# Kernel tuning notes

Hardware: AMD Instinct MI355X
Metric: run time of the kernel (lower is better)

## Reference

```python
import jax, jax.numpy as jnp
import numpy as np

TEMPERATURE = 1.0  # module default current_temperature
TOP_K = 2
NUM_EXPERTS = 64
EPS = 1e-10


def setup_inputs() -> dict:
    key = jax.random.key(0)
    k1, k2 = jax.random.split(key)
    x = jax.random.normal(k1, (4, 4096, 2048), dtype=jnp.float32)
    # nn.Linear(d_model, num_experts) weight has shape [num_experts, d_model]
    W_gate = jax.random.normal(k2, (NUM_EXPERTS, 2048), dtype=jnp.float32) * (1.0 / np.sqrt(2048))
    return {"x": x, "W_gate": W_gate}


def reference(x, W_gate):
    # Gate GEMM: [B,S,D] x [E,D] -> [B,S,E]
    logits = jnp.einsum("bsd,ed->bse", x, W_gate)
    scaled = logits / TEMPERATURE
    # Full distribution over experts (for load-balancing loss)
    router_probs = jax.nn.softmax(scaled, axis=-1)
    # Top-k selection over the expert dim, then renormalize via softmax
    top_k_logits, top_k_indices = jax.lax.top_k(scaled, TOP_K)  # [B,S,K]
    top_k_weights = jax.nn.softmax(top_k_logits, axis=-1)
    # Routing stats (no-grad in torch; plain values here)
    entropy = -jnp.sum(router_probs * jnp.log(router_probs + EPS), axis=-1)
    routing_entropy = entropy.mean()
    selection_confidence = top_k_weights[:, :, 0].mean()
    counts = jnp.zeros((NUM_EXPERTS,), dtype=x.dtype).at[top_k_indices.reshape(-1)].add(1.0)
    expert_utilization = counts / (counts.sum() + EPS)
    return (top_k_weights, top_k_indices, router_probs,
            routing_entropy, selection_confidence, expert_utilization)
```

## Files before the change

kernel.cpp:

```cpp
#include <hip/hip_runtime.h>
#include <math.h>

#define NTOK 16384
#define DIM 2048
#define NEXP 64
#define TB 32
#define NSTAGE 64

#define OFF_W    0
#define OFF_I    32768
#define OFF_P    65536
#define OFF_ENT  1114112
#define OFF_CONF 1114113
#define OFF_UTIL 1114114

typedef short s16x8 __attribute__((ext_vector_type(8)));
typedef float f32x4 __attribute__((ext_vector_type(4)));

__device__ __forceinline__ unsigned short f2bf(float v) {
    unsigned u = __builtin_bit_cast(unsigned, v);
    u = u + 0x7FFFu + ((u >> 16) & 1u);
    return (unsigned short)(u >> 16);
}
__device__ __forceinline__ float bf2f(unsigned short b) {
    return __builtin_bit_cast(float, (unsigned)b << 16);
}

__global__ void router_init(float* __restrict__ out) {
    int tid = threadIdx.x;
    if (tid < 66) out[OFF_ENT + tid] = 0.0f;
}

__global__ void router_wsplit(const float* __restrict__ Wg, uint4* __restrict__ wsp) {
    const int c = blockIdx.x;
    const int t = threadIdx.x;
    const int nt = t >> 6, l = t & 63;
    const int e  = 16 * nt + (l & 15);
    const int k0 = 32 * c + 8 * (l >> 4);
    const float* src = Wg + (size_t)e * DIM + k0;
    float4 a = *(const float4*)src;
    float4 b = *(const float4*)(src + 4);
    float v[8] = {a.x, a.y, a.z, a.w, b.x, b.y, b.z, b.w};
    unsigned short H[8], M[8], L[8];
    #pragma unroll
    for (int j = 0; j < 8; ++j) {
        H[j] = f2bf(v[j]);  float r = v[j] - bf2f(H[j]);
        M[j] = f2bf(r);     r = r - bf2f(M[j]);
        L[j] = f2bf(r);
    }
    uint4 ph, pm, pl;
    ph.x = H[0] | ((unsigned)H[1] << 16); ph.y = H[2] | ((unsigned)H[3] << 16);
    ph.z = H[4] | ((unsigned)H[5] << 16); ph.w = H[6] | ((unsigned)H[7] << 16);
    pm.x = M[0] | ((unsigned)M[1] << 16); pm.y = M[2] | ((unsigned)M[3] << 16);
    pm.z = M[4] | ((unsigned)M[5] << 16); pm.w = M[6] | ((unsigned)M[7] << 16);
    pl.x = L[0] | ((unsigned)L[1] << 16); pl.y = L[2] | ((unsigned)L[3] << 16);
    pl.z = L[4] | ((unsigned)L[5] << 16); pl.w = L[6] | ((unsigned)L[7] << 16);
    const int idx = c * 256 + t;
    wsp[idx]         = ph;
    wsp[16384 + idx] = pm;
    wsp[32768 + idx] = pl;
}

#define LOADW(W_, c_) { const int b_ = (c_)*256 + np*128 + l;  \
    W_[0] = wq[b_];          W_[1] = wq[b_ + 64];              \
    W_[2] = wq[16384 + b_];  W_[3] = wq[16384 + b_ + 64];      \
    W_[4] = wq[32768 + b_];  W_[5] = wq[32768 + b_ + 64]; }

#define SPLIT8(a0_, a1_, ph_, pm_, pl_) {                                \
    float xv[8] = {a0_.x, a0_.y, a0_.z, a0_.w,                           \
                   a1_.x, a1_.y, a1_.z, a1_.w};                          \
    unsigned hw_[8], mw_[8], lw_[8];                                     \
    _Pragma("unroll")                                                    \
    for (int j = 0; j < 8; ++j) {                                        \
        unsigned u_  = __builtin_bit_cast(unsigned, xv[j]);              \
        unsigned hb_ = u_ & 0xFFFF0000u;                                 \
        float    r_  = xv[j] - __builtin_bit_cast(float, hb_);           \
        unsigned mb_ = __builtin_bit_cast(unsigned, r_) & 0xFFFF0000u;   \
        float    r2_ = r_ - __builtin_bit_cast(float, mb_);              \
        unsigned lb_ = __builtin_bit_cast(unsigned, r2_);                \
        hw_[j] = hb_ >> 16; mw_[j] = mb_ >> 16; lw_[j] = lb_ >> 16;      \
    }                                                                    \
    ph_.x = hw_[0] | (hw_[1] << 16); ph_.y = hw_[2] | (hw_[3] << 16);    \
    ph_.z = hw_[4] | (hw_[5] << 16); ph_.w = hw_[6] | (hw_[7] << 16);    \
    pm_.x = mw_[0] | (mw_[1] << 16); pm_.y = mw_[2] | (mw_[3] << 16);    \
    pm_.z = mw_[4] | (mw_[5] << 16); pm_.w = mw_[6] | (mw_[7] << 16);    \
    pl_.x = lw_[0] | (lw_[1] << 16); pl_.y = lw_[2] | (lw_[3] << 16);    \
    pl_.z = lw_[4] | (lw_[5] << 16); pl_.w = lw_[6] | (lw_[7] << 16);    \
}

#define STAGEW(buf_) {                                                   \
    uint4 ph_, pm_, pl_;                                                 \
    SPLIT8(xr0, xr1, ph_, pm_, pl_);                                     \
    Xp[buf_][0][cc][st][sq] = ph_;                                       \
    Xp[buf_][1][cc][st][sq] = pm_;                                       \
    Xp[buf_][2][cc][st][sq] = pl_;                                       \
}

#define READA(buf_, cc_) {                                               \
    const int sl_ = qd ^ (tl & 3);                                       \
    ah = __builtin_bit_cast(s16x8, Xp[buf_][0][cc_][tl][sl_]);           \
    am = __builtin_bit_cast(s16x8, Xp[buf_][1][cc_][tl][sl_]);           \
    al = __builtin_bit_cast(s16x8, Xp[buf_][2][cc_][tl][sl_]);           \
}

#define COMPUTE(W_) {                                                    \
    s16x8 b0h_ = __builtin_bit_cast(s16x8, W_[0]);                       \
    s16x8 b1h_ = __builtin_bit_cast(s16x8, W_[1]);                       \
    s16x8 b0m_ = __builtin_bit_cast(s16x8, W_[2]);                       \
    s16x8 b1m_ = __builtin_bit_cast(s16x8, W_[3]);                       \
    s16x8 b0l_ = __builtin_bit_cast(s16x8, W_[4]);                       \
    s16x8 b1l_ = __builtin_bit_cast(s16x8, W_[5]);                       \
    acc0 = __builtin_amdgcn_mfma_f32_16x16x32_bf16(ah, b0h_, acc0, 0, 0, 0); \
    acc1 = __builtin_amdgcn_mfma_f32_16x16x32_bf16(ah, b1h_, acc1, 0, 0, 0); \
    acc0 = __builtin_amdgcn_mfma_f32_16x16x32_bf16(am, b0h_, acc0, 0, 0, 0); \
    acc1 = __builtin_amdgcn_mfma_f32_16x16x32_bf16(am, b1h_, acc1, 0, 0, 0); \
    acc0 = __builtin_amdgcn_mfma_f32_16x16x32_bf16(ah, b0m_, acc0, 0, 0, 0); \
    acc1 = __builtin_amdgcn_mfma_f32_16x16x32_bf16(ah, b1m_, acc1, 0, 0, 0); \
    acc0 = __builtin_amdgcn_mfma_f32_16x16x32_bf16(am, b0m_, acc0, 0, 0, 0); \
    acc1 = __builtin_amdgcn_mfma_f32_16x16x32_bf16(am, b1m_, acc1, 0, 0, 0); \
    acc0 = __builtin_amdgcn_mfma_f32_16x16x32_bf16(ah, b0l_, acc0, 0, 0, 0); \
    acc1 = __builtin_amdgcn_mfma_f32_16x16x32_bf16(ah, b1l_, acc1, 0, 0, 0); \
    acc0 = __builtin_amdgcn_mfma_f32_16x16x32_bf16(al, b0h_, acc0, 0, 0, 0); \
    acc1 = __builtin_amdgcn_mfma_f32_16x16x32_bf16(al, b1h_, acc1, 0, 0, 0); \
    }

__global__ __launch_bounds__(256, 2) void router_main(
    const float* __restrict__ x, const uint4* __restrict__ wq,
    float* __restrict__ out)
{
    __shared__ __align__(16) uint4 Xp[2][3][2][TB][4];
    __shared__ float lg[TB][NEXP + 1];
    __shared__ float m1s[TB], rss[TB];
    __shared__ float s_ent, s_conf, s_cnt[NEXP];

    const int tid = threadIdx.x;
    const int l   = tid & 63;
    const int w   = tid >> 6;
    const int np  = __builtin_amdgcn_readfirstlane(w >> 1);
    const int tt  = w & 1;
    const int qd  = l >> 4;
    const int tl  = tt * 16 + (l & 15);
    const int t0  = blockIdx.x * TB;

    if (tid == 0) { s_ent = 0.0f; s_conf = 0.0f; }
    if (tid < NEXP) s_cnt[tid] = 0.0f;

    const int cc  = tid >> 7;
    const int rr  = tid & 127;
    const int st  = rr >> 2;
    const int sq  = rr & 3;
    const int gq  = sq ^ (st & 3);
    const float* xsrc = x + (size_t)(t0 + st) * DIM + 8 * gq;

    f32x4 acc0 = (f32x4)(0.0f), acc1 = (f32x4)(0.0f);
    s16x8 ah, am, al;
    uint4 wA[6], wB[6];
    float4 xr0, xr1;

    xr0 = *(const float4*)(xsrc + cc * 32);
    xr1 = *(const float4*)(xsrc + cc * 32 + 4);
    LOADW(wA, 0); LOADW(wB, 1);
    STAGEW(0);
    xr0 = *(const float4*)(xsrc + (2 + cc) * 32);
    xr1 = *(const float4*)(xsrc + (2 + cc) * 32 + 4);
    __syncthreads();

    for (int s = 0; s < NSTAGE; s += 2) {
        const int buf = (s >> 1) & 1;
        if (s + 2 < NSTAGE) STAGEW(buf ^ 1);
        if (s + 4 < NSTAGE) {
            xr0 = *(const float4*)(xsrc + (s + 4 + cc) * 32);
            xr1 = *(const float4*)(xsrc + (s + 4 + cc) * 32 + 4);
        }
        READA(buf, 0);
        COMPUTE(wA);
        if (s + 2 < NSTAGE) LOADW(wA, s + 2);
        READA(buf, 1);
        COMPUTE(wB);
        if (s + 3 < NSTAGE) LOADW(wB, s + 3);
        asm volatile("s_waitcnt lgkmcnt(0)" ::: "memory");
        __builtin_amdgcn_sched_barrier(0);
        __builtin_amdgcn_s_barrier();
        __builtin_amdgcn_sched_barrier(0);
    }

    #pragma unroll
    for (int r = 0; r < 4; ++r) {
        lg[tt * 16 + 4 * qd + r][np * 32 + (l & 15)]      = acc0[r];
        lg[tt * 16 + 4 * qd + r][np * 32 + 16 + (l & 15)] = acc1[r];
    }
    __syncthreads();

    if (tid < TB) {
        const int t = tid;
        float m1 = -INFINITY, m2 = -INFINITY;
        int i1 = 0, i2 = 0;
        for (int e = 0; e < NEXP; ++e) {
            float lv = lg[t][e];
            if (lv > m1)      { m2 = m1; i2 = i1; m1 = lv; i1 = e; }
            else if (lv > m2) { m2 = lv; i2 = e; }
        }
        float ssum = 0.0f, tsum = 0.0f;
        for (int e = 0; e < NEXP; ++e) {
            float d = lg[t][e] - m1;
            float ex = __expf(d);
            ssum += ex;
            tsum += d * ex;
        }
        float rs = 1.0f / ssum;
        float H  = logf(ssum) - tsum * rs;
        float e2 = __expf(m2 - m1);
        float rn = 1.0f / (1.0f + e2);
        float w0 = rn, w1v = e2 * rn;
        m1s[t] = m1; rss[t] = rs;

        *(float2*)&out[OFF_W + 2 * (t0 + t)] = make_float2(w0, w1v);
        *(float2*)&out[OFF_I + 2 * (t0 + t)] = make_float2((float)i1, (float)i2);

        atomicAdd(&s_ent,  H);
        atomicAdd(&s_conf, w0);
        atomicAdd(&s_cnt[i1], 1.0f);
        atomicAdd(&s_cnt[i2], 1.0f);
    }
    __syncthreads();

    #pragma unroll
    for (int p = 0; p < 2; ++p) {
        int Q  = tid + 256 * p;
        int t  = Q >> 4;
        int qq = Q & 15;
        float m  = m1s[t];
        float rs = rss[t];
        float4 pr;
        pr.x = __expf(lg[t][4 * qq + 0] - m) * rs;
        pr.y = __expf(lg[t][4 * qq + 1] - m) * rs;
        pr.z = __expf(lg[t][4 * qq + 2] - m) * rs;
        pr.w = __expf(lg[t][4 * qq + 3] - m) * rs;
        *(float4*)&out[OFF_P + (size_t)(t0 + t) * NEXP + 4 * qq] = pr;
    }

    if (tid == 0) {
        atomicAdd(&out[OFF_ENT],  s_ent  * (1.0f / 16384.0f));
        atomicAdd(&out[OFF_CONF], s_conf * (1.0f / 16384.0f));
    }
    if (tid < NEXP)
        atomicAdd(&out[OFF_UTIL + tid], s_cnt[tid] * (1.0f / 32768.0f));
}

extern "C" void kernel_launch(void* const* d_in, const int* in_sizes, int n_in,
                              void* d_out, int out_size, void* d_ws, size_t ws_size,
                              hipStream_t stream) {
    const float* x  = (const float*)d_in[0];
    const float* Wg = (const float*)d_in[1];
    float* out = (float*)d_out;
    (void)in_sizes; (void)n_in; (void)out_size; (void)ws_size;

    router_init<<<dim3(1), dim3(128), 0, stream>>>(out);
    router_wsplit<<<dim3(NSTAGE), dim3(256), 0, stream>>>(Wg, (uint4*)d_ws);
    router_main<<<dim3(NTOK / TB), dim3(256), 0, stream>>>(x, (const uint4*)d_ws, out);
}
```

Baseline: 242.9 us.

## Split K dimension across two warp groups per block and fuse init kernel

Doubles the block to 512 threads, with two 256-thread groups each computing half of the 2048-wide reduction into separate shared staging buffers. The partial logits are summed through shared memory before the softmax/top-k epilogue. The output-zeroing kernel is folded into the weight-split kernel, removing one launch, and the LDS swizzle pattern is changed. This raises parallelism and latency hiding per token tile, at the cost of doubled shared staging memory and an extra reduction barrier.

```diff
diff --git a/kernel.cpp b/kernel.cpp
--- a/kernel.cpp
+++ b/kernel.cpp
@@ -5,7 +5,7 @@
 #define DIM 2048
 #define NEXP 64
 #define TB 32
-#define NSTAGE 64
+#define NSG 32
 
 #define OFF_W    0
 #define OFF_I    32768
@@ -26,14 +26,11 @@
     return __builtin_bit_cast(float, (unsigned)b << 16);
 }
 
-__global__ void router_init(float* __restrict__ out) {
-    int tid = threadIdx.x;
-    if (tid < 66) out[OFF_ENT + tid] = 0.0f;
-}
-
-__global__ void router_wsplit(const float* __restrict__ Wg, uint4* __restrict__ wsp) {
+__global__ void router_wsplit(const float* __restrict__ Wg, uint4* __restrict__ wsp,
+                              float* __restrict__ out) {
     const int c = blockIdx.x;
     const int t = threadIdx.x;
+    if (c == 0 && t < 66) out[OFF_ENT + t] = 0.0f;
     const int nt = t >> 6, l = t & 63;
     const int e  = 16 * nt + (l & 15);
     const int k0 = 32 * c + 8 * (l >> 4);
@@ -91,16 +88,15 @@
 #define STAGEW(buf_) {                                                   \
     uint4 ph_, pm_, pl_;                                                 \
     SPLIT8(xr0, xr1, ph_, pm_, pl_);                                     \
-    Xp[buf_][0][cc][st][sq] = ph_;                                       \
-    Xp[buf_][1][cc][st][sq] = pm_;                                       \
-    Xp[buf_][2][cc][st][sq] = pl_;                                       \
+    Xp[g][buf_][0][cc][st][sq] = ph_;                                    \
+    Xp[g][buf_][1][cc][st][sq] = pm_;                                    \
+    Xp[g][buf_][2][cc][st][sq] = pl_;                                    \
 }
 
 #define READA(buf_, cc_) {                                               \
-    const int sl_ = qd ^ (tl & 3);                                       \
-    ah = __builtin_bit_cast(s16x8, Xp[buf_][0][cc_][tl][sl_]);           \
-    am = __builtin_bit_cast(s16x8, Xp[buf_][1][cc_][tl][sl_]);           \
-    al = __builtin_bit_cast(s16x8, Xp[buf_][2][cc_][tl][sl_]);           \
+    ah = __builtin_bit_cast(s16x8, Xp[g][buf_][0][cc_][tl][sl]);         \
+    am = __builtin_bit_cast(s16x8, Xp[g][buf_][1][cc_][tl][sl]);         \
+    al = __builtin_bit_cast(s16x8, Xp[g][buf_][2][cc_][tl][sl]);         \
 }
 
 #define COMPUTE(W_) {                                                    \
@@ -124,11 +120,11 @@
     acc1 = __builtin_amdgcn_mfma_f32_16x16x32_bf16(al, b1h_, acc1, 0, 0, 0); \
     }
 
-__global__ __launch_bounds__(256, 2) void router_main(
+__global__ __launch_bounds__(512, 4) void router_main(
     const float* __restrict__ x, const uint4* __restrict__ wq,
     float* __restrict__ out)
 {
-    __shared__ __align__(16) uint4 Xp[2][3][2][TB][4];
+    __shared__ __align__(16) uint4 Xp[2][2][3][2][TB][4];
     __shared__ float lg[TB][NEXP + 1];
     __shared__ float m1s[TB], rss[TB];
     __shared__ float s_ent, s_conf, s_cnt[NEXP];
@@ -136,21 +132,26 @@
     const int tid = threadIdx.x;
     const int l   = tid & 63;
     const int w   = tid >> 6;
-    const int np  = __builtin_amdgcn_readfirstlane(w >> 1);
-    const int tt  = w & 1;
+    const int g   = tid >> 8;
+    const int lw  = w & 3;
+    const int np  = __builtin_amdgcn_readfirstlane(lw >> 1);
+    const int tt  = lw & 1;
     const int qd  = l >> 4;
     const int tl  = tt * 16 + (l & 15);
+    const int sl  = qd ^ ((tl >> 2) & 3);
     const int t0  = blockIdx.x * TB;
+    const int cb  = g * NSG;
 
     if (tid == 0) { s_ent = 0.0f; s_conf = 0.0f; }
     if (tid < NEXP) s_cnt[tid] = 0.0f;
 
-    const int cc  = tid >> 7;
-    const int rr  = tid & 127;
+    const int gtid = tid & 255;
+    const int cc  = gtid >> 7;
+    const int rr  = gtid & 127;
     const int st  = rr >> 2;
     const int sq  = rr & 3;
-    const int gq  = sq ^ (st & 3);
-    const float* xsrc = x + (size_t)(t0 + st) * DIM + 8 * gq;
+    const int gq  = sq ^ ((st >> 2) & 3);
+    const float* xsrc = x + (size_t)(t0 + st) * DIM + 32 * cb + 8 * gq;
 
     f32x4 acc0 = (f32x4)(0.0f), acc1 = (f32x4)(0.0f);
     s16x8 ah, am, al;
@@ -159,35 +160,45 @@
 
     xr0 = *(const float4*)(xsrc + cc * 32);
     xr1 = *(const float4*)(xsrc + cc * 32 + 4);
-    LOADW(wA, 0); LOADW(wB, 1);
+    LOADW(wA, cb + 0); LOADW(wB, cb + 1);
     STAGEW(0);
     xr0 = *(const float4*)(xsrc + (2 + cc) * 32);
     xr1 = *(const float4*)(xsrc + (2 + cc) * 32 + 4);
     __syncthreads();
 
-    for (int s = 0; s < NSTAGE; s += 2) {
+    for (int s = 0; s < NSG; s += 2) {
         const int buf = (s >> 1) & 1;
-        if (s + 2 < NSTAGE) STAGEW(buf ^ 1);
-        if (s + 4 < NSTAGE) {
+        if (s + 2 < NSG) STAGEW(buf ^ 1);
+        if (s + 4 < NSG) {
             xr0 = *(const float4*)(xsrc + (s + 4 + cc) * 32);
             xr1 = *(const float4*)(xsrc + (s + 4 + cc) * 32 + 4);
         }
         READA(buf, 0);
         COMPUTE(wA);
-        if (s + 2 < NSTAGE) LOADW(wA, s + 2);
+        if (s + 2 < NSG) LOADW(wA, cb + s + 2);
         READA(buf, 1);
         COMPUTE(wB);
-        if (s + 3 < NSTAGE) LOADW(wB, s + 3);
+        if (s + 3 < NSG) LOADW(wB, cb + s + 3);
         asm volatile("s_waitcnt lgkmcnt(0)" ::: "memory");
         __builtin_amdgcn_sched_barrier(0);
         __builtin_amdgcn_s_barrier();
         __builtin_amdgcn_sched_barrier(0);
     }
 
-    #pragma unroll
-    for (int r = 0; r < 4; ++r) {
-        lg[tt * 16 + 4 * qd + r][np * 32 + (l & 15)]      = acc0[r];
-        lg[tt * 16 + 4 * qd + r][np * 32 + 16 + (l & 15)] = acc1[r];
+    if (g == 1) {
+        #pragma unroll
+        for (int r = 0; r < 4; ++r) {
+            lg[tt * 16 + 4 * qd + r][np * 32 + (l & 15)]      = acc0[r];
+            lg[tt * 16 + 4 * qd + r][np * 32 + 16 + (l & 15)] = acc1[r];
+        }
+    }
+    __syncthreads();
+    if (g == 0) {
+        #pragma unroll
+        for (int r = 0; r < 4; ++r) {
+            lg[tt * 16 + 4 * qd + r][np * 32 + (l & 15)]      += acc0[r];
+            lg[tt * 16 + 4 * qd + r][np * 32 + 16 + (l & 15)] += acc1[r];
+        }
     }
     __syncthreads();
 
@@ -224,11 +235,9 @@
     }
     __syncthreads();
 
-    #pragma unroll
-    for (int p = 0; p < 2; ++p) {
-        int Q  = tid + 256 * p;
-        int t  = Q >> 4;
-        int qq = Q & 15;
+    {
+        int t  = tid >> 4;
+        int qq = tid & 15;
         float m  = m1s[t];
         float rs = rss[t];
         float4 pr;
@@ -255,7 +264,6 @@
     float* out = (float*)d_out;
     (void)in_sizes; (void)n_in; (void)out_size; (void)ws_size;
 
-    router_init<<<dim3(1), dim3(128), 0, stream>>>(out);
-    router_wsplit<<<dim3(NSTAGE), dim3(256), 0, stream>>>(Wg, (uint4*)d_ws);
-    router_main<<<dim3(NTOK / TB), dim3(256), 0, stream>>>(x, (const uint4*)d_ws, out);
-}
+    router_wsplit<<<dim3(64), dim3(256), 0, stream>>>(Wg, (uint4*)d_ws, out);
+    router_main<<<dim3(NTOK / TB), dim3(512), 0, stream>>>(x, (const uint4*)d_ws, out);
+}
```

New measurement: 231.2 us. 4.8% less time.
